# Performance work log

Measured on AMD Instinct MI355X. Metric: run time of the kernel, lower is better.

## Reference

```python
import jax, jax.numpy as jnp
import numpy as np

K = 0.5   # margin constant from __init__
T = 0.1   # temperature from __init__
EPS = 1e-8  # torch CosineSimilarity default eps

N_NODES, D_FEAT, N_TRIPLETS = 500_000, 64, 1_000_000


def setup_inputs() -> dict:
    key = jax.random.key(0)
    k1, k2 = jax.random.split(key)
    feats = jax.random.normal(k1, (N_NODES, D_FEAT), dtype=jnp.float32)
    # Precomputed triplets (anchor, positive, sampled negative) --
    # stands in for the data-dependent per-class sampling loop.
    tplts = jax.random.randint(k2, (3, N_TRIPLETS), 0, N_NODES, dtype=jnp.int64)
    return {"feats": feats, "tplts": tplts}


def _cosine(a, b):
    # torch.nn.CosineSimilarity(dim=1) semantics with eps clamp on norms
    num = jnp.sum(a * b, axis=-1)
    na = jnp.maximum(jnp.sqrt(jnp.sum(a * a, axis=-1)), EPS)
    nb = jnp.maximum(jnp.sqrt(jnp.sum(b * b, axis=-1)), EPS)
    return num / (na * nb)


def reference(feats, tplts):
    fa = feats[tplts[0]]          # [E, D] anchors
    fp = feats[tplts[1]]          # [E, D] positives
    fn = feats[tplts[2]]          # [E, D] negatives
    cs_ap = _cosine(fa, fp)
    cs_an = _cosine(fa, fn)
    # log1p(exp(x)) == softplus(x), numerically stable
    loss_ap = jax.nn.softplus(-(cs_ap - K) / T)
    loss_an = jax.nn.softplus((cs_an - K) / T)
    return (loss_ap + loss_an).mean()
```

## Files before the change

kernel.cpp:

```cpp
#include <hip/hip_runtime.h>
#include <math.h>


#define LSM_K 0.5f
#define LSM_INV_T 10.0f
#define LSM_EPS 1e-8f

__device__ __forceinline__ float softplus_f(float x) {
    return fmaxf(x, 0.0f) + log1pf(expf(-fabsf(x)));
}

__global__ __launch_bounds__(256) void lsm_loss_kernel(
    const float* __restrict__ feats,
    const int*   __restrict__ tplts,
    float*       __restrict__ out,
    int n_trip)
{
    const int lane = threadIdx.x & 63;
    const int gl   = threadIdx.x & 3;
    const int groups_per_block = blockDim.x >> 2;
    const int g_global = blockIdx.x * groups_per_block + (threadIdx.x >> 2);
    const int g_stride = gridDim.x * groups_per_block;

    const int* __restrict__ A  = tplts;
    const int* __restrict__ P  = tplts + n_trip;
    const int* __restrict__ Ng = tplts + 2 * n_trip;

    float local = 0.0f;

    for (int t = g_global; t < n_trip; t += g_stride) {
        const int ia  = A[t];
        const int ip  = P[t];
        const int in_ = Ng[t];

        const float4* __restrict__ ra = (const float4*)(feats + (size_t)ia  * 64);
        const float4* __restrict__ rp = (const float4*)(feats + (size_t)ip  * 64);
        const float4* __restrict__ rn = (const float4*)(feats + (size_t)in_ * 64);

        float s_ap = 0.0f, s_an = 0.0f, s_aa = 0.0f, s_pp = 0.0f, s_nn = 0.0f;

        #pragma unroll
        for (int c = 0; c < 4; ++c) {
            const float4 a = ra[c * 4 + gl];
            const float4 p = rp[c * 4 + gl];
            const float4 q = rn[c * 4 + gl];
            s_ap += a.x*p.x + a.y*p.y + a.z*p.z + a.w*p.w;
            s_an += a.x*q.x + a.y*q.y + a.z*q.z + a.w*q.w;
            s_aa += a.x*a.x + a.y*a.y + a.z*a.z + a.w*a.w;
            s_pp += p.x*p.x + p.y*p.y + p.z*p.z + p.w*p.w;
            s_nn += q.x*q.x + q.y*q.y + q.z*q.z + q.w*q.w;
        }

        #pragma unroll
        for (int m = 1; m < 4; m <<= 1) {
            s_ap += __shfl_xor(s_ap, m, 64);
            s_an += __shfl_xor(s_an, m, 64);
            s_aa += __shfl_xor(s_aa, m, 64);
            s_pp += __shfl_xor(s_pp, m, 64);
            s_nn += __shfl_xor(s_nn, m, 64);
        }

        if (gl == 0) {
            const float na = fmaxf(sqrtf(s_aa), LSM_EPS);
            const float np = fmaxf(sqrtf(s_pp), LSM_EPS);
            const float nn = fmaxf(sqrtf(s_nn), LSM_EPS);
            const float cs_ap = s_ap / (na * np);
            const float cs_an = s_an / (na * nn);
            local += softplus_f(-(cs_ap - LSM_K) * LSM_INV_T)
                   + softplus_f( (cs_an - LSM_K) * LSM_INV_T);
        }
    }

    float v = local;
    #pragma unroll
    for (int m = 4; m < 64; m <<= 1)
        v += __shfl_xor(v, m, 64);

    __shared__ float wave_sums[4];
    const int wave_id = threadIdx.x >> 6;
    if (lane == 0) wave_sums[wave_id] = v;
    __syncthreads();

    if (threadIdx.x == 0) {
        float s = wave_sums[0] + wave_sums[1] + wave_sums[2] + wave_sums[3];
        atomicAdd(out, s * (1.0f / (float)n_trip));
    }
}

extern "C" void kernel_launch(void* const* d_in, const int* in_sizes, int n_in,
                              void* d_out, int out_size, void* d_ws, size_t ws_size,
                              hipStream_t stream) {
    const float* feats = (const float*)d_in[0];
    const int*   tplts = (const int*)d_in[1];
    float*       out   = (float*)d_out;
    const int n_trip = in_sizes[1] / 3;

    hipMemsetAsync(out, 0, sizeof(float), stream);

    const dim3 block(256);
    const dim3 grid(2048);
    lsm_loss_kernel<<<grid, block, 0, stream>>>(feats, tplts, out, n_trip);
}
```

Measured before the change: 271.5 us.

## Pre-normalize features to fp16 and gather half-width rows with fdot2

Adds a pass that L2-normalizes every feature row once and stores it as fp16 in the workspace. The loss kernel then gathers these half-size rows, computes only the two cross dot products with packed fp16 dot instructions, and drops the per-triplet norm computation. The aim is to halve the random-gather traffic, which dominates the cost, and to remove redundant norm work. In exchange it adds a full read and write of the feature table every call and loses precision through fp16 rounding. It falls back to the fp32 kernel when the workspace is too small.

New measurement: 252.2 us. 1.08x faster.

```diff
diff --git a/kernel.cpp b/kernel.cpp
--- a/kernel.cpp
+++ b/kernel.cpp
@@ -5,12 +5,123 @@
 #define LSM_K 0.5f
 #define LSM_INV_T 10.0f
 #define LSM_EPS 1e-8f
+#define N_FEAT 64
+
+typedef _Float16 half2_t __attribute__((ext_vector_type(2)));
+typedef _Float16 half4_t __attribute__((ext_vector_type(4)));
 
 __device__ __forceinline__ float softplus_f(float x) {
     return fmaxf(x, 0.0f) + log1pf(expf(-fabsf(x)));
 }
 
-__global__ __launch_bounds__(256) void lsm_loss_kernel(
+__device__ __forceinline__ half2_t as_h2(unsigned u) {
+    return __builtin_bit_cast(half2_t, u);
+}
+
+__global__ __launch_bounds__(256) void normalize_f16_kernel(
+    const float* __restrict__ feats,
+    _Float16*    __restrict__ nfeats,
+    int n_rows)
+{
+    const int gl = threadIdx.x & 15;
+    const int r0 = (int)((blockIdx.x * blockDim.x + threadIdx.x) >> 4);
+    const int rstride = (int)((gridDim.x * blockDim.x) >> 4);
+
+    for (int r = r0; r < n_rows; r += rstride) {
+        const float4 v = ((const float4*)(feats + (size_t)r * N_FEAT))[gl];
+        float s = v.x*v.x + v.y*v.y + v.z*v.z + v.w*v.w;
+        #pragma unroll
+        for (int m = 1; m < 16; m <<= 1)
+            s += __shfl_xor(s, m, 64);
+        const float scale = 1.0f / fmaxf(sqrtf(s), LSM_EPS);
+        half4_t h;
+        h.x = (_Float16)(v.x * scale);
+        h.y = (_Float16)(v.y * scale);
+        h.z = (_Float16)(v.z * scale);
+        h.w = (_Float16)(v.w * scale);
+        ((half4_t*)(nfeats + (size_t)r * N_FEAT))[gl] = h;
+    }
+}
+
+__global__ __launch_bounds__(256) void lsm_loss_f16_kernel(
+    const _Float16* __restrict__ nfeats,
+    const int*      __restrict__ tplts,
+    float*          __restrict__ out,
+    int n_trip)
+{
+    const int lane = threadIdx.x & 63;
+    const int gl   = threadIdx.x & 3;
+    const int groups_per_block = blockDim.x >> 2;
+    const int g_global = blockIdx.x * groups_per_block + (threadIdx.x >> 2);
+    const int g_stride = gridDim.x * groups_per_block;
+
+    const int* __restrict__ A  = tplts;
+    const int* __restrict__ P  = tplts + n_trip;
+    const int* __restrict__ Ng = tplts + 2 * n_trip;
+
+    float local = 0.0f;
+
+    for (int t = g_global; t < n_trip; t += g_stride) {
+        const int ia  = A[t];
+        const int ip  = P[t];
+        const int in_ = Ng[t];
+
+        const uint4* __restrict__ ra = (const uint4*)(nfeats + (size_t)ia  * N_FEAT);
+        const uint4* __restrict__ rp = (const uint4*)(nfeats + (size_t)ip  * N_FEAT);
+        const uint4* __restrict__ rn = (const uint4*)(nfeats + (size_t)in_ * N_FEAT);
+
+        const uint4 a0 = ra[gl], a1 = ra[4 + gl];
+        const uint4 p0 = rp[gl], p1 = rp[4 + gl];
+        const uint4 q0 = rn[gl], q1 = rn[4 + gl];
+
+        float s_ap = 0.0f, s_an = 0.0f;
+        s_ap = __builtin_amdgcn_fdot2(as_h2(a0.x), as_h2(p0.x), s_ap, false);
+        s_ap = __builtin_amdgcn_fdot2(as_h2(a0.y), as_h2(p0.y), s_ap, false);
+        s_ap = __builtin_amdgcn_fdot2(as_h2(a0.z), as_h2(p0.z), s_ap, false);
+        s_ap = __builtin_amdgcn_fdot2(as_h2(a0.w), as_h2(p0.w), s_ap, false);
+        s_ap = __builtin_amdgcn_fdot2(as_h2(a1.x), as_h2(p1.x), s_ap, false);
+        s_ap = __builtin_amdgcn_fdot2(as_h2(a1.y), as_h2(p1.y), s_ap, false);
+        s_ap = __builtin_amdgcn_fdot2(as_h2(a1.z), as_h2(p1.z), s_ap, false);
+        s_ap = __builtin_amdgcn_fdot2(as_h2(a1.w), as_h2(p1.w), s_ap, false);
+
+        s_an = __builtin_amdgcn_fdot2(as_h2(a0.x), as_h2(q0.x), s_an, false);
+        s_an = __builtin_amdgcn_fdot2(as_h2(a0.y), as_h2(q0.y), s_an, false);
+        s_an = __builtin_amdgcn_fdot2(as_h2(a0.z), as_h2(q0.z), s_an, false);
+        s_an = __builtin_amdgcn_fdot2(as_h2(a0.w), as_h2(q0.w), s_an, false);
+        s_an = __builtin_amdgcn_fdot2(as_h2(a1.x), as_h2(q1.x), s_an, false);
+        s_an = __builtin_amdgcn_fdot2(as_h2(a1.y), as_h2(q1.y), s_an, false);
+        s_an = __builtin_amdgcn_fdot2(as_h2(a1.z), as_h2(q1.z), s_an, false);
+        s_an = __builtin_amdgcn_fdot2(as_h2(a1.w), as_h2(q1.w), s_an, false);
+
+        #pragma unroll
+        for (int m = 1; m < 4; m <<= 1) {
+            s_ap += __shfl_xor(s_ap, m, 64);
+            s_an += __shfl_xor(s_an, m, 64);
+        }
+
+        if (gl == 0) {
+            local += softplus_f(-(s_ap - LSM_K) * LSM_INV_T)
+                   + softplus_f( (s_an - LSM_K) * LSM_INV_T);
+        }
+    }
+
+    float v = local;
+    #pragma unroll
+    for (int m = 4; m < 64; m <<= 1)
+        v += __shfl_xor(v, m, 64);
+
+    __shared__ float wave_sums[4];
+    const int wave_id = threadIdx.x >> 6;
+    if (lane == 0) wave_sums[wave_id] = v;
+    __syncthreads();
+
+    if (threadIdx.x == 0) {
+        float s = wave_sums[0] + wave_sums[1] + wave_sums[2] + wave_sums[3];
+        atomicAdd(out, s * (1.0f / (float)n_trip));
+    }
+}
+
+__global__ __launch_bounds__(256) void lsm_loss_f32_kernel(
     const float* __restrict__ feats,
     const int*   __restrict__ tplts,
     float*       __restrict__ out,
@@ -27,30 +138,20 @@
     const int* __restrict__ Ng = tplts + 2 * n_trip;
 
     float local = 0.0f;
-
     for (int t = g_global; t < n_trip; t += g_stride) {
-        const int ia  = A[t];
-        const int ip  = P[t];
-        const int in_ = Ng[t];
-
-        const float4* __restrict__ ra = (const float4*)(feats + (size_t)ia  * 64);
-        const float4* __restrict__ rp = (const float4*)(feats + (size_t)ip  * 64);
-        const float4* __restrict__ rn = (const float4*)(feats + (size_t)in_ * 64);
-
-        float s_ap = 0.0f, s_an = 0.0f, s_aa = 0.0f, s_pp = 0.0f, s_nn = 0.0f;
-
+        const float4* ra = (const float4*)(feats + (size_t)A[t]  * N_FEAT);
+        const float4* rp = (const float4*)(feats + (size_t)P[t]  * N_FEAT);
+        const float4* rn = (const float4*)(feats + (size_t)Ng[t] * N_FEAT);
+        float s_ap = 0, s_an = 0, s_aa = 0, s_pp = 0, s_nn = 0;
         #pragma unroll
         for (int c = 0; c < 4; ++c) {
-            const float4 a = ra[c * 4 + gl];
-            const float4 p = rp[c * 4 + gl];
-            const float4 q = rn[c * 4 + gl];
+            const float4 a = ra[c*4+gl], p = rp[c*4+gl], q = rn[c*4+gl];
             s_ap += a.x*p.x + a.y*p.y + a.z*p.z + a.w*p.w;
             s_an += a.x*q.x + a.y*q.y + a.z*q.z + a.w*q.w;
             s_aa += a.x*a.x + a.y*a.y + a.z*a.z + a.w*a.w;
             s_pp += p.x*p.x + p.y*p.y + p.z*p.z + p.w*p.w;
             s_nn += q.x*q.x + q.y*q.y + q.z*q.z + q.w*q.w;
         }
-
         #pragma unroll
         for (int m = 1; m < 4; m <<= 1) {
             s_ap += __shfl_xor(s_ap, m, 64);
@@ -59,28 +160,20 @@
             s_pp += __shfl_xor(s_pp, m, 64);
             s_nn += __shfl_xor(s_nn, m, 64);
         }
-
         if (gl == 0) {
             const float na = fmaxf(sqrtf(s_aa), LSM_EPS);
             const float np = fmaxf(sqrtf(s_pp), LSM_EPS);
             const float nn = fmaxf(sqrtf(s_nn), LSM_EPS);
-            const float cs_ap = s_ap / (na * np);
-            const float cs_an = s_an / (na * nn);
-            local += softplus_f(-(cs_ap - LSM_K) * LSM_INV_T)
-                   + softplus_f( (cs_an - LSM_K) * LSM_INV_T);
-        }
-    }
-
+            local += softplus_f(-(s_ap/(na*np) - LSM_K) * LSM_INV_T)
+                   + softplus_f( (s_an/(na*nn) - LSM_K) * LSM_INV_T);
+        }
+    }
     float v = local;
     #pragma unroll
-    for (int m = 4; m < 64; m <<= 1)
-        v += __shfl_xor(v, m, 64);
-
+    for (int m = 4; m < 64; m <<= 1) v += __shfl_xor(v, m, 64);
     __shared__ float wave_sums[4];
-    const int wave_id = threadIdx.x >> 6;
-    if (lane == 0) wave_sums[wave_id] = v;
+    if (lane == 0) wave_sums[threadIdx.x >> 6] = v;
     __syncthreads();
-
     if (threadIdx.x == 0) {
         float s = wave_sums[0] + wave_sums[1] + wave_sums[2] + wave_sums[3];
         atomicAdd(out, s * (1.0f / (float)n_trip));
@@ -94,10 +187,19 @@
     const int*   tplts = (const int*)d_in[1];
     float*       out   = (float*)d_out;
     const int n_trip = in_sizes[1] / 3;
+    const int n_rows = in_sizes[0] / N_FEAT;
 
     hipMemsetAsync(out, 0, sizeof(float), stream);
 
-    const dim3 block(256);
-    const dim3 grid(2048);
-    lsm_loss_kernel<<<grid, block, 0, stream>>>(feats, tplts, out, n_trip);
-}
+    const size_t needed = (size_t)n_rows * N_FEAT * sizeof(_Float16);
+    if (ws_size >= needed) {
+        _Float16* nfeats = (_Float16*)d_ws;
+        normalize_f16_kernel<<<dim3((n_rows * 16 + 255) / 256), dim3(256), 0, stream>>>(
+            feats, nfeats, n_rows);
+        lsm_loss_f16_kernel<<<dim3(2048), dim3(256), 0, stream>>>(
+            nfeats, tplts, out, n_trip);
+    } else {
+        lsm_loss_f32_kernel<<<dim3(2048), dim3(256), 0, stream>>>(
+            feats, tplts, out, n_trip);
+    }
+}
```
